# Performance work log

Measured on AMD Instinct MI355X. Metric: run time of the kernel, lower is better.

Reference implementation:

```python
import jax, jax.numpy as jnp
import numpy as np

D_MODEL = 1024
NUM_HEADS = 16
HEAD_DIM = D_MODEL // NUM_HEADS  # 64
THETA = 10000.0
B, S = 2, 2048


def setup_inputs() -> dict:
    key = jax.random.key(0)
    k1, k2, k3 = jax.random.split(key, 3)
    sigma_qkv = (2.0 / (D_MODEL + 3 * D_MODEL)) ** 0.5
    sigma_o = (2.0 / (D_MODEL + D_MODEL)) ** 0.5
    x = jax.random.normal(k1, (B, S, D_MODEL), dtype=jnp.float32)
    w_qkv = jax.random.normal(k2, (3 * D_MODEL, D_MODEL), dtype=jnp.float32) * sigma_qkv
    w_o = jax.random.normal(k3, (D_MODEL, D_MODEL), dtype=jnp.float32) * sigma_o
    token_positions = jnp.arange(S, dtype=jnp.int32)
    return {"x": x, "w_qkv": w_qkv, "w_o": w_o, "token_positions": token_positions, "mask": 1}


def _rope(t, pos):
    # t: (B, H, S, HEAD_DIM); pos: (S,) int
    ids = jnp.arange(HEAD_DIM // 2, dtype=jnp.float32)
    freqs = pos.astype(jnp.float32)[:, None] * (THETA ** (-2.0 * ids / HEAD_DIM))  # (S, HEAD_DIM/2)
    cos, sin = jnp.cos(freqs), jnp.sin(freqs)
    even, odd = t[..., 0::2], t[..., 1::2]
    r_even = even * cos - odd * sin
    r_odd = odd * cos + even * sin
    # interleave back to original layout
    return jnp.stack([r_even, r_odd], axis=-1).reshape(t.shape)


def reference(x, w_qkv, w_o, token_positions, mask):
    # fused QKV projection: Linear computes x @ W^T with W [out, in]
    qkv = x @ w_qkv.T  # (B, S, 3*D_MODEL)
    q, k, v = jnp.split(qkv, 3, axis=-1)

    def to_heads(t):
        return t.reshape(B, S, NUM_HEADS, HEAD_DIM).transpose(0, 2, 1, 3)  # (B, H, S, Dh)

    q, k, v = to_heads(q), to_heads(k), to_heads(v)
    q = _rope(q, token_positions)
    k = _rope(k, token_positions)

    scores = jnp.einsum('bhqd,bhkd->bhqk', q, k)
    if mask:  # causal: lower-triangular allowed
        causal = jnp.tril(jnp.ones((S, S), dtype=bool))
        scores = jnp.where(causal, scores, -jnp.inf)
    attn = jax.nn.softmax(scores * (HEAD_DIM ** -0.5), axis=-1)
    out = jnp.einsum('bhqk,bhkd->bhqd', attn, v)  # (B, H, S, Dh)
    out = out.transpose(0, 2, 1, 3).reshape(B, S, D_MODEL)
    return out @ w_o.T
```

## Files before the change

### kernel.cpp

```cpp
#include <hip/hip_runtime.h>
#include <hip/hip_bf16.h>
#include <math.h>

typedef __bf16 bf16_t;
typedef __bf16 bf16x8 __attribute__((ext_vector_type(8)));
typedef __bf16 bf16x4 __attribute__((ext_vector_type(4)));
typedef float  f32x4  __attribute__((ext_vector_type(4)));

#define D_MODEL 1024
#define NH      16
#define HD      64
#define BATCH   2
#define SEQ     2048
#define MROWS   (BATCH*SEQ)
#define QKVN    (3*D_MODEL)
#define FA_PAD  72
#define SCALE_LOG2E 0.18033688011112042f

__device__ __forceinline__ void async_cp16(const bf16_t* g, bf16_t* l) {
    __builtin_amdgcn_global_load_lds(
        (const __attribute__((address_space(1))) void*)g,
        (__attribute__((address_space(3))) void*)l,
        16, 0, 0);
}

__global__ void cvt_all(const float* __restrict__ x, const float* __restrict__ wq,
                        const float* __restrict__ wo,
                        bf16_t* __restrict__ xb, bf16_t* __restrict__ wqb,
                        bf16_t* __restrict__ wob) {
    const int nx = MROWS * D_MODEL, nq = QKVN * D_MODEL;
    int i = (blockIdx.x * blockDim.x + threadIdx.x) * 4;
    const float* s; bf16_t* d; int off;
    if (i < nx)           { s = x;  d = xb;  off = i; }
    else if (i < nx + nq) { s = wq; d = wqb; off = i - nx; }
    else                  { s = wo; d = wob; off = i - nx - nq; }
    float4 v = *(const float4*)(s + off);
    d[off]     = (bf16_t)v.x;
    d[off + 1] = (bf16_t)v.y;
    d[off + 2] = (bf16_t)v.z;
    d[off + 3] = (bf16_t)v.w;
}

template <typename OutT, int NI>
__global__ __launch_bounds__(256) void gemm_nt(const bf16_t* __restrict__ A,
                                               const bf16_t* __restrict__ Bm,
                                               OutT* __restrict__ C,
                                               int M, int N, int K) {
    __shared__ __align__(16) bf16_t As[128 * 32];
    __shared__ __align__(16) bf16_t Bs[NI * 32 * 32];
    const int tid  = threadIdx.x;
    const int w    = tid >> 6;
    const int lane = tid & 63;
    const int quad = lane >> 4;
    const int l16  = lane & 15;
    const int m0   = blockIdx.x * 128;
    const int n0   = blockIdx.y * (NI * 32);
    const int wm   = (w >> 1) * 64;
    const int wn   = (w & 1) * (NI * 16);

    f32x4 acc[4][NI];
    #pragma unroll
    for (int i = 0; i < 4; i++)
        #pragma unroll
        for (int j = 0; j < NI; j++)
            acc[i][j] = (f32x4){0.f, 0.f, 0.f, 0.f};

    const bf16_t* Ag0 = A  + (size_t)(m0 + (tid >> 2)) * K + (tid & 3) * 8;
    const bf16_t* Ag1 = Ag0 + (size_t)64 * K;
    const bf16_t* Bg0 = Bm + (size_t)(n0 + (tid >> 2)) * K + (tid & 3) * 8;
    const bf16_t* Bg1 = Bg0 + (size_t)64 * K;
    bf16_t* Al0 = &As[(size_t)tid * 8];
    bf16_t* Al1 = &As[((size_t)tid + 256) * 8];
    bf16_t* Bl0 = &Bs[(size_t)tid * 8];
    bf16_t* Bl1 = &Bs[((size_t)tid + 256) * 8];

    for (int k0 = 0; k0 < K; k0 += 32) {
        async_cp16(Ag0 + k0, Al0);
        async_cp16(Ag1 + k0, Al1);
        async_cp16(Bg0 + k0, Bl0);
        if (NI == 4) async_cp16(Bg1 + k0, Bl1);
        __syncthreads();

        bf16x8 af[4], bfr[NI];
        #pragma unroll
        for (int mi = 0; mi < 4; mi++)
            af[mi] = *(const bf16x8*)&As[(wm + mi * 16 + l16) * 32 + quad * 8];
        #pragma unroll
        for (int ni = 0; ni < NI; ni++)
            bfr[ni] = *(const bf16x8*)&Bs[(wn + ni * 16 + l16) * 32 + quad * 8];
        #pragma unroll
        for (int mi = 0; mi < 4; mi++)
            #pragma unroll
            for (int ni = 0; ni < NI; ni++)
                acc[mi][ni] = __builtin_amdgcn_mfma_f32_16x16x32_bf16(
                    af[mi], bfr[ni], acc[mi][ni], 0, 0, 0);
        __syncthreads();
    }

    #pragma unroll
    for (int mi = 0; mi < 4; mi++)
        #pragma unroll
        for (int ni = 0; ni < NI; ni++) {
            const int col = n0 + wn + ni * 16 + l16;
            #pragma unroll
            for (int r = 0; r < 4; r++) {
                const int row = m0 + wm + mi * 16 + quad * 4 + r;
                C[(size_t)row * N + col] = (OutT)acc[mi][ni][r];
            }
        }
}

__global__ __launch_bounds__(256) void rope_split(const bf16_t* __restrict__ qkv,
                                                  const int* __restrict__ pos,
                                                  bf16_t* __restrict__ Qh,
                                                  bf16_t* __restrict__ Kh,
                                                  bf16_t* __restrict__ VT) {
    __shared__ bf16_t vs[128][FA_PAD];
    const int tid   = threadIdx.x;
    const int s_loc = tid >> 1;
    const int half  = tid & 1;
    const int s0    = blockIdx.x * 128;
    const int bh    = blockIdx.y;
    const int b     = bh >> 4, h = bh & 15;
    const int s     = s0 + s_loc;

    const bf16_t* row = qkv + (size_t)(b * SEQ + s) * QKVN + h * HD + half * 32;

    bf16_t qbuf[32], kbuf[32], vbuf[32];
    #pragma unroll
    for (int j = 0; j < 4; j++) {
        *(bf16x8*)&qbuf[j * 8] = *(const bf16x8*)(row + j * 8);
        *(bf16x8*)&kbuf[j * 8] = *(const bf16x8*)(row + D_MODEL + j * 8);
        *(bf16x8*)&vbuf[j * 8] = *(const bf16x8*)(row + 2 * D_MODEL + j * 8);
    }

    const float pf = (float)pos[s];
    #pragma unroll
    for (int p = 0; p < 16; p++) {
        const int d2 = half * 16 + p;
        const float inv = __expf(-0.28782313662425575f * (float)d2);
        const float f = pf * inv;
        const float c = cosf(f), sn = sinf(f);
        float qe = (float)qbuf[2 * p], qo = (float)qbuf[2 * p + 1];
        float ke = (float)kbuf[2 * p], ko = (float)kbuf[2 * p + 1];
        qbuf[2 * p]     = (bf16_t)(qe * c - qo * sn);
        qbuf[2 * p + 1] = (bf16_t)(qo * c + qe * sn);
        kbuf[2 * p]     = (bf16_t)(ke * c - ko * sn);
        kbuf[2 * p + 1] = (bf16_t)(ko * c + ke * sn);
    }

    bf16_t* qdst = Qh + ((size_t)bh * SEQ + s) * HD + half * 32;
    bf16_t* kdst = Kh + ((size_t)bh * SEQ + s) * HD + half * 32;
    #pragma unroll
    for (int j = 0; j < 4; j++) {
        *(bf16x8*)(qdst + j * 8) = *(bf16x8*)&qbuf[j * 8];
        *(bf16x8*)(kdst + j * 8) = *(bf16x8*)&kbuf[j * 8];
        *(bf16x8*)&vs[s_loc][half * 32 + j * 8] = *(bf16x8*)&vbuf[j * 8];
    }
    __syncthreads();

    const int d  = tid >> 2;
    const int sc = tid & 3;
    bf16_t tmp[32];
    #pragma unroll
    for (int i = 0; i < 32; i++) tmp[i] = vs[sc * 32 + i][d];
    bf16_t* vdst = VT + ((size_t)bh * HD + d) * SEQ + s0 + sc * 32;
    #pragma unroll
    for (int j = 0; j < 4; j++)
        *(bf16x8*)(vdst + j * 8) = *(bf16x8*)&tmp[j * 8];
}

__global__ __launch_bounds__(512) void flash_attn(const bf16_t* __restrict__ Qh,
                                                  const bf16_t* __restrict__ Kh,
                                                  const bf16_t* __restrict__ VT,
                                                  bf16_t* __restrict__ AO) {
    __shared__ __align__(16) bf16_t Ks[2][64 * FA_PAD];
    __shared__ __align__(16) bf16_t Vs[2][64 * FA_PAD];
    __shared__ __align__(16) bf16_t pT[8][16][FA_PAD];

    const int tid  = threadIdx.x;
    const int w    = tid >> 6;
    const int lane = tid & 63;
    const int quad = lane >> 4;
    const int l16  = lane & 15;
    const int wq   = w & 3;
    const int g    = w >> 2;

    const int bid  = blockIdx.x;
    const int xcd  = bid & 7;
    const int mm   = bid >> 3;
    const int bh   = (mm >> 4) * 8 + xcd;
    const int pair = mm & 15;
    const int qt_big = 31 - pair;
    const int my_qt  = g ? pair : qt_big;
    const int niter  = qt_big + 1;

    const bf16_t* Qb = Qh + (size_t)bh * SEQ * HD;
    const bf16_t* Kb = Kh + (size_t)bh * SEQ * HD;
    const bf16_t* Vb = VT + (size_t)bh * HD * SEQ;

    const int q0 = my_qt * 64 + wq * 16;
    const bf16x8 aq0 = *(const bf16x8*)(Qb + (size_t)(q0 + l16) * HD + quad * 8);
    const bf16x8 aq1 = *(const bf16x8*)(Qb + (size_t)(q0 + l16) * HD + 32 + quad * 8);

    const int srow = tid >> 3, scol = (tid & 7) * 8;
    const int lds_off = srow * FA_PAD + scol;

    f32x4 o[4];
    #pragma unroll
    for (int i = 0; i < 4; i++) o[i] = (f32x4){0.f, 0.f, 0.f, 0.f};
    float lsum = 0.f;

    bf16x8 pK = *(const bf16x8*)(Kb + (size_t)srow * HD + scol);
    bf16x8 pV = *(const bf16x8*)(Vb + (size_t)srow * SEQ + scol);
    *(bf16x8*)&Ks[0][lds_off] = pK;
    *(bf16x8*)&Vs[0][lds_off] = pV;

    for (int kt = 0; kt < niter; ++kt) {
        const int cur = kt & 1;
        if (kt + 1 < niter) {
            const int kn = (kt + 1) * 64;
            pK = *(const bf16x8*)(Kb + (size_t)(kn + srow) * HD + scol);
            pV = *(const bf16x8*)(Vb + (size_t)srow * SEQ + kn + scol);
        }
        __syncthreads();

        if (kt <= my_qt) {
            const bool diag = (kt == my_qt);
            const bf16_t* KsC = &Ks[cur][0];
            const bf16_t* VsC = &Vs[cur][0];

            #pragma unroll
            for (int ni = 0; ni < 4; ni++) {
                if (diag && ni > wq) {
                    *(bf16x4*)&pT[w][l16][ni * 16 + quad * 4] = (bf16x4){0, 0, 0, 0};
                    continue;
                }
                bf16x8 kb0 = *(const bf16x8*)&KsC[(ni * 16 + l16) * FA_PAD + quad * 8];
                bf16x8 kb1 = *(const bf16x8*)&KsC[(ni * 16 + l16) * FA_PAD + 32 + quad * 8];
                f32x4 t = (f32x4){0.f, 0.f, 0.f, 0.f};
                t = __builtin_amdgcn_mfma_f32_16x16x32_bf16(kb0, aq0, t, 0, 0, 0);
                t = __builtin_amdgcn_mfma_f32_16x16x32_bf16(kb1, aq1, t, 0, 0, 0);
                bf16x4 pk;
                #pragma unroll
                for (int r = 0; r < 4; r++) {
                    float pv = exp2f(t[r] * SCALE_LOG2E);
                    if (diag && (ni * 16 + quad * 4 + r > wq * 16 + l16)) pv = 0.f;
                    lsum += pv;
                    pk[r] = (bf16_t)pv;
                }
                *(bf16x4*)&pT[w][l16][ni * 16 + quad * 4] = pk;
            }

            #pragma unroll
            for (int ks = 0; ks < 2; ks++) {
                if (diag && wq * 16 + 15 < ks * 32) continue;
                bf16x8 ap = *(const bf16x8*)&pT[w][l16][ks * 32 + quad * 8];
                #pragma unroll
                for (int ni = 0; ni < 4; ni++) {
                    bf16x8 vb = *(const bf16x8*)&VsC[(ni * 16 + l16) * FA_PAD + ks * 32 + quad * 8];
                    o[ni] = __builtin_amdgcn_mfma_f32_16x16x32_bf16(ap, vb, o[ni], 0, 0, 0);
                }
            }
        }

        if (kt + 1 < niter) {
            *(bf16x8*)&Ks[cur ^ 1][lds_off] = pK;
            *(bf16x8*)&Vs[cur ^ 1][lds_off] = pV;
        }
    }

    lsum += __shfl_xor(lsum, 16);
    lsum += __shfl_xor(lsum, 32);
    f32x4 linv;
    #pragma unroll
    for (int r = 0; r < 4; r++)
        linv[r] = 1.0f / __shfl(lsum, quad * 4 + r);

    const int b = bh >> 4, h = bh & 15;
    #pragma unroll
    for (int ni = 0; ni < 4; ni++) {
        #pragma unroll
        for (int r = 0; r < 4; r++) {
            const size_t row = (size_t)b * SEQ + q0 + quad * 4 + r;
            AO[row * D_MODEL + h * HD + ni * 16 + l16] = (bf16_t)(o[ni][r] * linv[r]);
        }
    }
}

extern "C" void kernel_launch(void* const* d_in, const int* in_sizes, int n_in,
                              void* d_out, int out_size, void* d_ws, size_t ws_size,
                              hipStream_t stream) {
    const float* x     = (const float*)d_in[0];
    const float* w_qkv = (const float*)d_in[1];
    const float* w_o   = (const float*)d_in[2];
    const int*   tpos  = (const int*)d_in[3];
    float*       out   = (float*)d_out;

    char* ws = (char*)d_ws;
    bf16_t* xb  = (bf16_t*)(ws);
    bf16_t* wqb = (bf16_t*)(ws + 8388608);
    bf16_t* wob = (bf16_t*)(ws + 14680064);
    bf16_t* qkv = (bf16_t*)(ws + 16777216);
    bf16_t* Qh  = (bf16_t*)(ws + 41943040);
    bf16_t* Kh  = (bf16_t*)(ws + 50331648);
    bf16_t* VT  = (bf16_t*)(ws + 58720256);
    bf16_t* AO  = (bf16_t*)(ws + 67108864);

    cvt_all<<<8192, 256, 0, stream>>>(x, w_qkv, w_o, xb, wqb, wob);

    gemm_nt<bf16_t, 4><<<dim3(32, 24), 256, 0, stream>>>(xb, wqb, qkv, MROWS, QKVN, D_MODEL);

    rope_split<<<dim3(SEQ / 128, BATCH * NH), 256, 0, stream>>>(qkv, tpos, Qh, Kh, VT);

    flash_attn<<<512, 512, 0, stream>>>(Qh, Kh, VT, AO);

    gemm_nt<float, 2><<<dim3(32, 16), 256, 0, stream>>>(AO, wob, out, MROWS, D_MODEL, D_MODEL);
}
```

Measured before the change: 201.8 us.

## Split each attention query tile's KV range across two wave groups and merge

Each block now owns a single 64-row query tile, and the two 4-wave groups each process half of the causal KV range. Partial output and row sums are merged through LDS at the end. The old scheme paired a large and a small query tile in one block, so one group often sat idle. The grid doubles to 1024 blocks and the block-to-head mapping changes, at the cost of an extra LDS reduction, an added barrier per iteration, and losing the cross-iteration prefetch double-buffer. Softmax still omits a running max, which is safe only because the two partial sums share no max to rescale.

```diff
diff --git a/kernel.cpp b/kernel.cpp
--- a/kernel.cpp
+++ b/kernel.cpp
@@ -187,19 +187,23 @@
     const int g    = w >> 2;
 
     const int bid  = blockIdx.x;
-    const int xcd  = bid & 7;
-    const int mm   = bid >> 3;
-    const int bh   = (mm >> 4) * 8 + xcd;
-    const int pair = mm & 15;
-    const int qt_big = 31 - pair;
-    const int my_qt  = g ? pair : qt_big;
-    const int niter  = qt_big + 1;
+    const int bh   = bid & 31;
+    const int tb   = bid >> 5;
+    const int u    = tb & 7;
+    const int qtr  = tb >> 3;
+    const int my_t = (qtr == 0) ? (31 - u)
+                   : (qtr == 1) ? (16 + u)
+                   : (qtr == 2) ? (15 - u) : u;
+
+    const int nkv   = my_t + 1;
+    const int h     = nkv >> 1;
+    const int niter = nkv - h;
 
     const bf16_t* Qb = Qh + (size_t)bh * SEQ * HD;
     const bf16_t* Kb = Kh + (size_t)bh * SEQ * HD;
     const bf16_t* Vb = VT + (size_t)bh * HD * SEQ;
 
-    const int q0 = my_qt * 64 + wq * 16;
+    const int q0 = my_t * 64 + wq * 16;
     const bf16x8 aq0 = *(const bf16x8*)(Qb + (size_t)(q0 + l16) * HD + quad * 8);
     const bf16x8 aq1 = *(const bf16x8*)(Qb + (size_t)(q0 + l16) * HD + 32 + quad * 8);
 
@@ -211,24 +215,39 @@
     for (int i = 0; i < 4; i++) o[i] = (f32x4){0.f, 0.f, 0.f, 0.f};
     float lsum = 0.f;
 
-    bf16x8 pK = *(const bf16x8*)(Kb + (size_t)srow * HD + scol);
-    bf16x8 pV = *(const bf16x8*)(Vb + (size_t)srow * SEQ + scol);
-    *(bf16x8*)&Ks[0][lds_off] = pK;
-    *(bf16x8*)&Vs[0][lds_off] = pV;
-
-    for (int kt = 0; kt < niter; ++kt) {
-        const int cur = kt & 1;
-        if (kt + 1 < niter) {
-            const int kn = (kt + 1) * 64;
-            pK = *(const bf16x8*)(Kb + (size_t)(kn + srow) * HD + scol);
-            pV = *(const bf16x8*)(Vb + (size_t)srow * SEQ + kn + scol);
-        }
+    bf16x8 pK0, pV0, pK1, pV1;
+    if (h > 0) {
+        pK0 = *(const bf16x8*)(Kb + (size_t)srow * HD + scol);
+        pV0 = *(const bf16x8*)(Vb + (size_t)srow * SEQ + scol);
+    }
+    pK1 = *(const bf16x8*)(Kb + (size_t)(h * 64 + srow) * HD + scol);
+    pV1 = *(const bf16x8*)(Vb + (size_t)srow * SEQ + h * 64 + scol);
+
+    for (int i = 0; i < niter; ++i) {
+        if (i < h) {
+            *(bf16x8*)&Ks[0][lds_off] = pK0;
+            *(bf16x8*)&Vs[0][lds_off] = pV0;
+        }
+        *(bf16x8*)&Ks[1][lds_off] = pK1;
+        *(bf16x8*)&Vs[1][lds_off] = pV1;
         __syncthreads();
 
-        if (kt <= my_qt) {
-            const bool diag = (kt == my_qt);
-            const bf16_t* KsC = &Ks[cur][0];
-            const bf16_t* VsC = &Vs[cur][0];
+        if (i + 1 < niter) {
+            if (i + 1 < h) {
+                const int k0n = (i + 1) * 64;
+                pK0 = *(const bf16x8*)(Kb + (size_t)(k0n + srow) * HD + scol);
+                pV0 = *(const bf16x8*)(Vb + (size_t)srow * SEQ + k0n + scol);
+            }
+            const int k1n = (h + i + 1) * 64;
+            pK1 = *(const bf16x8*)(Kb + (size_t)(k1n + srow) * HD + scol);
+            pV1 = *(const bf16x8*)(Vb + (size_t)srow * SEQ + k1n + scol);
+        }
+
+        const bool active = g ? true : (i < h);
+        if (active) {
+            const bool diag = g && (i == niter - 1);
+            const bf16_t* KsC = &Ks[g][0];
+            const bf16_t* VsC = &Vs[g][0];
 
             #pragma unroll
             for (int ni = 0; ni < 4; ni++) {
@@ -263,27 +282,39 @@
                 }
             }
         }
-
-        if (kt + 1 < niter) {
-            *(bf16x8*)&Ks[cur ^ 1][lds_off] = pK;
-            *(bf16x8*)&Vs[cur ^ 1][lds_off] = pV;
-        }
-    }
-
-    lsum += __shfl_xor(lsum, 16);
-    lsum += __shfl_xor(lsum, 32);
-    f32x4 linv;
-    #pragma unroll
-    for (int r = 0; r < 4; r++)
-        linv[r] = 1.0f / __shfl(lsum, quad * 4 + r);
-
-    const int b = bh >> 4, h = bh & 15;
-    #pragma unroll
-    for (int ni = 0; ni < 4; ni++) {
-        #pragma unroll
-        for (int r = 0; r < 4; r++) {
-            const size_t row = (size_t)b * SEQ + q0 + quad * 4 + r;
-            AO[row * D_MODEL + h * HD + ni * 16 + l16] = (bf16_t)(o[ni][r] * linv[r]);
+        __syncthreads();
+    }
+
+    f32x4* mo = (f32x4*)&Ks[0][0];
+    float* ml = (float*)(mo + 256 * 4);
+    if (g) {
+        const int base = (wq * 64 + lane) * 4;
+        #pragma unroll
+        for (int ni = 0; ni < 4; ni++) mo[base + ni] = o[ni];
+        ml[wq * 64 + lane] = lsum;
+    }
+    __syncthreads();
+    if (!g) {
+        const int base = (wq * 64 + lane) * 4;
+        #pragma unroll
+        for (int ni = 0; ni < 4; ni++) o[ni] += mo[base + ni];
+        lsum += ml[wq * 64 + lane];
+
+        lsum += __shfl_xor(lsum, 16);
+        lsum += __shfl_xor(lsum, 32);
+        f32x4 linv;
+        #pragma unroll
+        for (int r = 0; r < 4; r++)
+            linv[r] = 1.0f / __shfl(lsum, quad * 4 + r);
+
+        const int b = bh >> 4, hh = bh & 15;
+        #pragma unroll
+        for (int ni = 0; ni < 4; ni++) {
+            #pragma unroll
+            for (int r = 0; r < 4; r++) {
+                const size_t row = (size_t)b * SEQ + q0 + quad * 4 + r;
+                AO[row * D_MODEL + hh * HD + ni * 16 + l16] = (bf16_t)(o[ni][r] * linv[r]);
+            }
         }
     }
 }
@@ -313,7 +344,7 @@
 
     rope_split<<<dim3(SEQ / 128, BATCH * NH), 256, 0, stream>>>(qkv, tpos, Qh, Kh, VT);
 
-    flash_attn<<<512, 512, 0, stream>>>(Qh, Kh, VT, AO);
+    flash_attn<<<1024, 512, 0, stream>>>(Qh, Kh, VT, AO);
 
     gemm_nt<float, 2><<<dim3(32, 16), 256, 0, stream>>>(AO, wob, out, MROWS, D_MODEL, D_MODEL);
 }
```

Measured after the change: 197.0 us. -2.4%, faster.

## Restructure flash attention: per-wave 32-row Q tiles, direct global K/V loads, no block sync

Applied to the files above, without the earlier changes.

The flash attention kernel drops the shared-memory double-buffered K/V tiles and block-wide barriers. Each wave now owns two 16-row query subtiles (32 rows) and reads K and V fragments straight from global memory, relying on L2/cache reuse. Waves in a block get query tiles chosen to balance causal work, and the grid shrinks from 512 to 256 blocks. Removing the barriers lets waves run independently, at the cost of redundant global loads per wave and lower block-level parallelism.

```diff
diff --git a/kernel.cpp b/kernel.cpp
--- a/kernel.cpp
+++ b/kernel.cpp
@@ -174,116 +174,145 @@
                                                   const bf16_t* __restrict__ Kh,
                                                   const bf16_t* __restrict__ VT,
                                                   bf16_t* __restrict__ AO) {
-    __shared__ __align__(16) bf16_t Ks[2][64 * FA_PAD];
-    __shared__ __align__(16) bf16_t Vs[2][64 * FA_PAD];
-    __shared__ __align__(16) bf16_t pT[8][16][FA_PAD];
+    __shared__ __align__(16) bf16_t pT[16][16][FA_PAD];
 
     const int tid  = threadIdx.x;
     const int w    = tid >> 6;
     const int lane = tid & 63;
     const int quad = lane >> 4;
     const int l16  = lane & 15;
-    const int wq   = w & 3;
-    const int g    = w >> 2;
 
     const int bid  = blockIdx.x;
-    const int xcd  = bid & 7;
-    const int mm   = bid >> 3;
-    const int bh   = (mm >> 4) * 8 + xcd;
-    const int pair = mm & 15;
-    const int qt_big = 31 - pair;
-    const int my_qt  = g ? pair : qt_big;
-    const int niter  = qt_big + 1;
+    const int bh   = bid & 31;
+    const int j    = bid >> 5;
+
+    int p;
+    switch (w) {
+        case 0: p = j;      break;
+        case 1: p = 15 - j; break;
+        case 2: p = 16 + j; break;
+        case 3: p = 31 - j; break;
+        case 4: p = 63 - j; break;
+        case 5: p = 48 + j; break;
+        case 6: p = 47 - j; break;
+        default: p = 32 + j;
+    }
+    const int q0   = p * 32;
+    const int nkv  = (q0 + 31) / 64 + 1;
 
     const bf16_t* Qb = Qh + (size_t)bh * SEQ * HD;
     const bf16_t* Kb = Kh + (size_t)bh * SEQ * HD;
     const bf16_t* Vb = VT + (size_t)bh * HD * SEQ;
 
-    const int q0 = my_qt * 64 + wq * 16;
-    const bf16x8 aq0 = *(const bf16x8*)(Qb + (size_t)(q0 + l16) * HD + quad * 8);
-    const bf16x8 aq1 = *(const bf16x8*)(Qb + (size_t)(q0 + l16) * HD + 32 + quad * 8);
-
-    const int srow = tid >> 3, scol = (tid & 7) * 8;
-    const int lds_off = srow * FA_PAD + scol;
-
-    f32x4 o[4];
-    #pragma unroll
-    for (int i = 0; i < 4; i++) o[i] = (f32x4){0.f, 0.f, 0.f, 0.f};
-    float lsum = 0.f;
-
-    bf16x8 pK = *(const bf16x8*)(Kb + (size_t)srow * HD + scol);
-    bf16x8 pV = *(const bf16x8*)(Vb + (size_t)srow * SEQ + scol);
-    *(bf16x8*)&Ks[0][lds_off] = pK;
-    *(bf16x8*)&Vs[0][lds_off] = pV;
-
-    for (int kt = 0; kt < niter; ++kt) {
-        const int cur = kt & 1;
-        if (kt + 1 < niter) {
-            const int kn = (kt + 1) * 64;
-            pK = *(const bf16x8*)(Kb + (size_t)(kn + srow) * HD + scol);
-            pV = *(const bf16x8*)(Vb + (size_t)srow * SEQ + kn + scol);
-        }
-        __syncthreads();
-
-        if (kt <= my_qt) {
-            const bool diag = (kt == my_qt);
-            const bf16_t* KsC = &Ks[cur][0];
-            const bf16_t* VsC = &Vs[cur][0];
-
-            #pragma unroll
-            for (int ni = 0; ni < 4; ni++) {
-                if (diag && ni > wq) {
-                    *(bf16x4*)&pT[w][l16][ni * 16 + quad * 4] = (bf16x4){0, 0, 0, 0};
-                    continue;
-                }
-                bf16x8 kb0 = *(const bf16x8*)&KsC[(ni * 16 + l16) * FA_PAD + quad * 8];
-                bf16x8 kb1 = *(const bf16x8*)&KsC[(ni * 16 + l16) * FA_PAD + 32 + quad * 8];
-                f32x4 t = (f32x4){0.f, 0.f, 0.f, 0.f};
-                t = __builtin_amdgcn_mfma_f32_16x16x32_bf16(kb0, aq0, t, 0, 0, 0);
-                t = __builtin_amdgcn_mfma_f32_16x16x32_bf16(kb1, aq1, t, 0, 0, 0);
-                bf16x4 pk;
-                #pragma unroll
-                for (int r = 0; r < 4; r++) {
-                    float pv = exp2f(t[r] * SCALE_LOG2E);
-                    if (diag && (ni * 16 + quad * 4 + r > wq * 16 + l16)) pv = 0.f;
-                    lsum += pv;
-                    pk[r] = (bf16_t)pv;
-                }
-                *(bf16x4*)&pT[w][l16][ni * 16 + quad * 4] = pk;
-            }
-
-            #pragma unroll
-            for (int ks = 0; ks < 2; ks++) {
-                if (diag && wq * 16 + 15 < ks * 32) continue;
-                bf16x8 ap = *(const bf16x8*)&pT[w][l16][ks * 32 + quad * 8];
+    bf16x8 aq[2][2];
+    #pragma unroll
+    for (int sub = 0; sub < 2; sub++) {
+        aq[sub][0] = *(const bf16x8*)(Qb + (size_t)(q0 + sub * 16 + l16) * HD + quad * 8);
+        aq[sub][1] = *(const bf16x8*)(Qb + (size_t)(q0 + sub * 16 + l16) * HD + 32 + quad * 8);
+    }
+
+    f32x4 o[2][4];
+    #pragma unroll
+    for (int sub = 0; sub < 2; sub++)
+        #pragma unroll
+        for (int i = 0; i < 4; i++) o[sub][i] = (f32x4){0.f, 0.f, 0.f, 0.f};
+    float lsum[2] = {0.f, 0.f};
+
+    for (int kt = 0; kt < nkv; ++kt) {
+        const int kbase = kt * 64;
+
+        bf16x8 kb[4][2];
+        #pragma unroll
+        for (int ni = 0; ni < 4; ni++) {
+            const bf16_t* kr = Kb + (size_t)(kbase + ni * 16 + l16) * HD + quad * 8;
+            kb[ni][0] = *(const bf16x8*)kr;
+            kb[ni][1] = *(const bf16x8*)(kr + 32);
+        }
+
+        const bool full = (kbase + 63 <= q0);
+        if (full) {
+            #pragma unroll
+            for (int sub = 0; sub < 2; sub++) {
+                const int wp = w * 2 + sub;
                 #pragma unroll
                 for (int ni = 0; ni < 4; ni++) {
-                    bf16x8 vb = *(const bf16x8*)&VsC[(ni * 16 + l16) * FA_PAD + ks * 32 + quad * 8];
-                    o[ni] = __builtin_amdgcn_mfma_f32_16x16x32_bf16(ap, vb, o[ni], 0, 0, 0);
+                    f32x4 t = (f32x4){0.f, 0.f, 0.f, 0.f};
+                    t = __builtin_amdgcn_mfma_f32_16x16x32_bf16(kb[ni][0], aq[sub][0], t, 0, 0, 0);
+                    t = __builtin_amdgcn_mfma_f32_16x16x32_bf16(kb[ni][1], aq[sub][1], t, 0, 0, 0);
+                    bf16x4 pk;
+                    #pragma unroll
+                    for (int r = 0; r < 4; r++) {
+                        float pv = exp2f(t[r] * SCALE_LOG2E);
+                        lsum[sub] += pv;
+                        pk[r] = (bf16_t)pv;
+                    }
+                    *(bf16x4*)&pT[wp][l16][ni * 16 + quad * 4] = pk;
                 }
             }
-        }
-
-        if (kt + 1 < niter) {
-            *(bf16x8*)&Ks[cur ^ 1][lds_off] = pK;
-            *(bf16x8*)&Vs[cur ^ 1][lds_off] = pV;
-        }
-    }
-
-    lsum += __shfl_xor(lsum, 16);
-    lsum += __shfl_xor(lsum, 32);
-    f32x4 linv;
-    #pragma unroll
-    for (int r = 0; r < 4; r++)
-        linv[r] = 1.0f / __shfl(lsum, quad * 4 + r);
-
-    const int b = bh >> 4, h = bh & 15;
-    #pragma unroll
-    for (int ni = 0; ni < 4; ni++) {
-        #pragma unroll
-        for (int r = 0; r < 4; r++) {
-            const size_t row = (size_t)b * SEQ + q0 + quad * 4 + r;
-            AO[row * D_MODEL + h * HD + ni * 16 + l16] = (bf16_t)(o[ni][r] * linv[r]);
+        } else {
+            #pragma unroll
+            for (int sub = 0; sub < 2; sub++) {
+                const int wp   = w * 2 + sub;
+                const int qmax = q0 + sub * 16 + 15;
+                const int qg   = q0 + sub * 16 + l16;
+                #pragma unroll
+                for (int ni = 0; ni < 4; ni++) {
+                    if (kbase + ni * 16 > qmax) {
+                        *(bf16x4*)&pT[wp][l16][ni * 16 + quad * 4] = (bf16x4){0, 0, 0, 0};
+                        continue;
+                    }
+                    f32x4 t = (f32x4){0.f, 0.f, 0.f, 0.f};
+                    t = __builtin_amdgcn_mfma_f32_16x16x32_bf16(kb[ni][0], aq[sub][0], t, 0, 0, 0);
+                    t = __builtin_amdgcn_mfma_f32_16x16x32_bf16(kb[ni][1], aq[sub][1], t, 0, 0, 0);
+                    bf16x4 pk;
+                    #pragma unroll
+                    for (int r = 0; r < 4; r++) {
+                        const int kvg = kbase + ni * 16 + quad * 4 + r;
+                        float pv = exp2f(t[r] * SCALE_LOG2E);
+                        if (kvg > qg) pv = 0.f;
+                        lsum[sub] += pv;
+                        pk[r] = (bf16_t)pv;
+                    }
+                    *(bf16x4*)&pT[wp][l16][ni * 16 + quad * 4] = pk;
+                }
+            }
+        }
+
+        #pragma unroll
+        for (int ks = 0; ks < 2; ks++) {
+            if (!full && kbase + ks * 32 > q0 + 31) continue;
+            bf16x8 vb[4];
+            #pragma unroll
+            for (int ni = 0; ni < 4; ni++)
+                vb[ni] = *(const bf16x8*)(Vb + (size_t)(ni * 16 + l16) * SEQ + kbase + ks * 32 + quad * 8);
+            #pragma unroll
+            for (int sub = 0; sub < 2; sub++) {
+                if (!full && kbase + ks * 32 > q0 + sub * 16 + 15) continue;
+                bf16x8 ap = *(const bf16x8*)&pT[w * 2 + sub][l16][ks * 32 + quad * 8];
+                #pragma unroll
+                for (int ni = 0; ni < 4; ni++)
+                    o[sub][ni] = __builtin_amdgcn_mfma_f32_16x16x32_bf16(ap, vb[ni], o[sub][ni], 0, 0, 0);
+            }
+        }
+    }
+
+    const int b = bh >> 4, hh = bh & 15;
+    #pragma unroll
+    for (int sub = 0; sub < 2; sub++) {
+        float ls = lsum[sub];
+        ls += __shfl_xor(ls, 16);
+        ls += __shfl_xor(ls, 32);
+        f32x4 linv;
+        #pragma unroll
+        for (int r = 0; r < 4; r++)
+            linv[r] = 1.0f / __shfl(ls, quad * 4 + r);
+        #pragma unroll
+        for (int ni = 0; ni < 4; ni++) {
+            #pragma unroll
+            for (int r = 0; r < 4; r++) {
+                const size_t row = (size_t)b * SEQ + q0 + sub * 16 + quad * 4 + r;
+                AO[row * D_MODEL + hh * HD + ni * 16 + l16] = (bf16_t)(o[sub][ni][r] * linv[r]);
+            }
         }
     }
 }
@@ -313,7 +342,7 @@
 
     rope_split<<<dim3(SEQ / 128, BATCH * NH), 256, 0, stream>>>(qkv, tpos, Qh, Kh, VT);
 
-    flash_attn<<<512, 512, 0, stream>>>(Qh, Kh, VT, AO);
+    flash_attn<<<256, 512, 0, stream>>>(Qh, Kh, VT, AO);
 
     gemm_nt<float, 2><<<dim3(32, 16), 256, 0, stream>>>(AO, wob, out, MROWS, D_MODEL, D_MODEL);
 }
```

New measurement: 230.2 us. 14.1% more time.

## Split paired-tile flash attention into single-tile 256-thread blocks with single-buffered LDS

Applied to the files above, without the earlier changes.

Each flash-attention block previously held 8 waves working on two query tiles (a long and a short one) that shared K/V loads through a double-buffered LDS ring. It now uses 4 waves per block, one query tile per block, and 1024 blocks ordered from longest to shortest tile. K/V use a single LDS buffer with register prefetch and two barriers per iteration. The aim is to remove the idle waves of the short tile in the paired scheme and to improve occupancy and load balance. In exchange, K/V are loaded from global memory more often and each iteration has an extra barrier.

```diff
diff --git a/kernel.cpp b/kernel.cpp
--- a/kernel.cpp
+++ b/kernel.cpp
@@ -170,104 +170,103 @@
         *(bf16x8*)(vdst + j * 8) = *(bf16x8*)&tmp[j * 8];
 }
 
-__global__ __launch_bounds__(512) void flash_attn(const bf16_t* __restrict__ Qh,
+__global__ __launch_bounds__(256) void flash_attn(const bf16_t* __restrict__ Qh,
                                                   const bf16_t* __restrict__ Kh,
                                                   const bf16_t* __restrict__ VT,
                                                   bf16_t* __restrict__ AO) {
-    __shared__ __align__(16) bf16_t Ks[2][64 * FA_PAD];
-    __shared__ __align__(16) bf16_t Vs[2][64 * FA_PAD];
-    __shared__ __align__(16) bf16_t pT[8][16][FA_PAD];
+    __shared__ __align__(16) bf16_t Ks[64 * FA_PAD];
+    __shared__ __align__(16) bf16_t Vs[64 * FA_PAD];
+    __shared__ __align__(16) bf16_t pT[4][16][FA_PAD];
 
     const int tid  = threadIdx.x;
     const int w    = tid >> 6;
     const int lane = tid & 63;
     const int quad = lane >> 4;
     const int l16  = lane & 15;
-    const int wq   = w & 3;
-    const int g    = w >> 2;
 
     const int bid  = blockIdx.x;
-    const int xcd  = bid & 7;
-    const int mm   = bid >> 3;
-    const int bh   = (mm >> 4) * 8 + xcd;
-    const int pair = mm & 15;
-    const int qt_big = 31 - pair;
-    const int my_qt  = g ? pair : qt_big;
-    const int niter  = qt_big + 1;
+    const int bh   = bid & 31;
+    const int tb   = bid >> 5;
+    const int u    = tb & 7;
+    const int qtr  = tb >> 3;
+    const int my_t = (qtr == 0) ? (31 - u)
+                   : (qtr == 1) ? (16 + u)
+                   : (qtr == 2) ? (15 - u) : u;
+    const int nkv  = my_t + 1;
 
     const bf16_t* Qb = Qh + (size_t)bh * SEQ * HD;
     const bf16_t* Kb = Kh + (size_t)bh * SEQ * HD;
     const bf16_t* Vb = VT + (size_t)bh * HD * SEQ;
 
-    const int q0 = my_qt * 64 + wq * 16;
+    const int q0 = my_t * 64 + w * 16;
     const bf16x8 aq0 = *(const bf16x8*)(Qb + (size_t)(q0 + l16) * HD + quad * 8);
     const bf16x8 aq1 = *(const bf16x8*)(Qb + (size_t)(q0 + l16) * HD + 32 + quad * 8);
 
     const int srow = tid >> 3, scol = (tid & 7) * 8;
-    const int lds_off = srow * FA_PAD + scol;
+    const int lds0 = srow * FA_PAD + scol;
+    const int lds1 = (srow + 32) * FA_PAD + scol;
 
     f32x4 o[4];
     #pragma unroll
     for (int i = 0; i < 4; i++) o[i] = (f32x4){0.f, 0.f, 0.f, 0.f};
     float lsum = 0.f;
 
-    bf16x8 pK = *(const bf16x8*)(Kb + (size_t)srow * HD + scol);
-    bf16x8 pV = *(const bf16x8*)(Vb + (size_t)srow * SEQ + scol);
-    *(bf16x8*)&Ks[0][lds_off] = pK;
-    *(bf16x8*)&Vs[0][lds_off] = pV;
-
-    for (int kt = 0; kt < niter; ++kt) {
-        const int cur = kt & 1;
-        if (kt + 1 < niter) {
+    bf16x8 pK0 = *(const bf16x8*)(Kb + (size_t)srow * HD + scol);
+    bf16x8 pK1 = *(const bf16x8*)(Kb + (size_t)(srow + 32) * HD + scol);
+    bf16x8 pV0 = *(const bf16x8*)(Vb + (size_t)srow * SEQ + scol);
+    bf16x8 pV1 = *(const bf16x8*)(Vb + (size_t)(srow + 32) * SEQ + scol);
+
+    for (int kt = 0; kt < nkv; ++kt) {
+        *(bf16x8*)&Ks[lds0] = pK0;
+        *(bf16x8*)&Ks[lds1] = pK1;
+        *(bf16x8*)&Vs[lds0] = pV0;
+        *(bf16x8*)&Vs[lds1] = pV1;
+        __syncthreads();
+
+        if (kt + 1 < nkv) {
             const int kn = (kt + 1) * 64;
-            pK = *(const bf16x8*)(Kb + (size_t)(kn + srow) * HD + scol);
-            pV = *(const bf16x8*)(Vb + (size_t)srow * SEQ + kn + scol);
-        }
-        __syncthreads();
-
-        if (kt <= my_qt) {
-            const bool diag = (kt == my_qt);
-            const bf16_t* KsC = &Ks[cur][0];
-            const bf16_t* VsC = &Vs[cur][0];
-
+            pK0 = *(const bf16x8*)(Kb + (size_t)(kn + srow) * HD + scol);
+            pK1 = *(const bf16x8*)(Kb + (size_t)(kn + srow + 32) * HD + scol);
+            pV0 = *(const bf16x8*)(Vb + (size_t)srow * SEQ + kn + scol);
+            pV1 = *(const bf16x8*)(Vb + (size_t)(srow + 32) * SEQ + kn + scol);
+        }
+
+        const bool diag = (kt == my_t);
+
+        #pragma unroll
+        for (int ni = 0; ni < 4; ni++) {
+            if (diag && ni > w) {
+                *(bf16x4*)&pT[w][l16][ni * 16 + quad * 4] = (bf16x4){0, 0, 0, 0};
+                continue;
+            }
+            bf16x8 kb0 = *(const bf16x8*)&Ks[(ni * 16 + l16) * FA_PAD + quad * 8];
+            bf16x8 kb1 = *(const bf16x8*)&Ks[(ni * 16 + l16) * FA_PAD + 32 + quad * 8];
+            f32x4 t = (f32x4){0.f, 0.f, 0.f, 0.f};
+            t = __builtin_amdgcn_mfma_f32_16x16x32_bf16(kb0, aq0, t, 0, 0, 0);
+            t = __builtin_amdgcn_mfma_f32_16x16x32_bf16(kb1, aq1, t, 0, 0, 0);
+            bf16x4 pk;
+            #pragma unroll
+            for (int r = 0; r < 4; r++) {
+                float pv = exp2f(t[r] * SCALE_LOG2E);
+                if (diag && (ni * 16 + quad * 4 + r > w * 16 + l16)) pv = 0.f;
+                lsum += pv;
+                pk[r] = (bf16_t)pv;
+            }
+            *(bf16x4*)&pT[w][l16][ni * 16 + quad * 4] = pk;
+        }
+
+        #pragma unroll
+        for (int ks = 0; ks < 2; ks++) {
+            if (diag && w * 16 + 15 < ks * 32) continue;
+            bf16x8 ap = *(const bf16x8*)&pT[w][l16][ks * 32 + quad * 8];
             #pragma unroll
             for (int ni = 0; ni < 4; ni++) {
-                if (diag && ni > wq) {
-                    *(bf16x4*)&pT[w][l16][ni * 16 + quad * 4] = (bf16x4){0, 0, 0, 0};
-                    continue;
-                }
-                bf16x8 kb0 = *(const bf16x8*)&KsC[(ni * 16 + l16) * FA_PAD + quad * 8];
-                bf16x8 kb1 = *(const bf16x8*)&KsC[(ni * 16 + l16) * FA_PAD + 32 + quad * 8];
-                f32x4 t = (f32x4){0.f, 0.f, 0.f, 0.f};
-                t = __builtin_amdgcn_mfma_f32_16x16x32_bf16(kb0, aq0, t, 0, 0, 0);
-                t = __builtin_amdgcn_mfma_f32_16x16x32_bf16(kb1, aq1, t, 0, 0, 0);
-                bf16x4 pk;
-                #pragma unroll
-                for (int r = 0; r < 4; r++) {
-                    float pv = exp2f(t[r] * SCALE_LOG2E);
-                    if (diag && (ni * 16 + quad * 4 + r > wq * 16 + l16)) pv = 0.f;
-                    lsum += pv;
-                    pk[r] = (bf16_t)pv;
-                }
-                *(bf16x4*)&pT[w][l16][ni * 16 + quad * 4] = pk;
+                bf16x8 vb = *(const bf16x8*)&Vs[(ni * 16 + l16) * FA_PAD + ks * 32 + quad * 8];
+                o[ni] = __builtin_amdgcn_mfma_f32_16x16x32_bf16(ap, vb, o[ni], 0, 0, 0);
             }
-
-            #pragma unroll
-            for (int ks = 0; ks < 2; ks++) {
-                if (diag && wq * 16 + 15 < ks * 32) continue;
-                bf16x8 ap = *(const bf16x8*)&pT[w][l16][ks * 32 + quad * 8];
-                #pragma unroll
-                for (int ni = 0; ni < 4; ni++) {
-                    bf16x8 vb = *(const bf16x8*)&VsC[(ni * 16 + l16) * FA_PAD + ks * 32 + quad * 8];
-                    o[ni] = __builtin_amdgcn_mfma_f32_16x16x32_bf16(ap, vb, o[ni], 0, 0, 0);
-                }
-            }
-        }
-
-        if (kt + 1 < niter) {
-            *(bf16x8*)&Ks[cur ^ 1][lds_off] = pK;
-            *(bf16x8*)&Vs[cur ^ 1][lds_off] = pV;
-        }
+        }
+
+        __syncthreads();
     }
 
     lsum += __shfl_xor(lsum, 16);
@@ -277,13 +276,13 @@
     for (int r = 0; r < 4; r++)
         linv[r] = 1.0f / __shfl(lsum, quad * 4 + r);
 
-    const int b = bh >> 4, h = bh & 15;
+    const int b = bh >> 4, hh = bh & 15;
     #pragma unroll
     for (int ni = 0; ni < 4; ni++) {
         #pragma unroll
         for (int r = 0; r < 4; r++) {
             const size_t row = (size_t)b * SEQ + q0 + quad * 4 + r;
-            AO[row * D_MODEL + h * HD + ni * 16 + l16] = (bf16_t)(o[ni][r] * linv[r]);
+            AO[row * D_MODEL + hh * HD + ni * 16 + l16] = (bf16_t)(o[ni][r] * linv[r]);
         }
     }
 }
@@ -313,7 +312,7 @@
 
     rope_split<<<dim3(SEQ / 128, BATCH * NH), 256, 0, stream>>>(qkv, tpos, Qh, Kh, VT);
 
-    flash_attn<<<512, 512, 0, stream>>>(Qh, Kh, VT, AO);
+    flash_attn<<<1024, 256, 0, stream>>>(Qh, Kh, VT, AO);
 
     gemm_nt<float, 2><<<dim3(32, 16), 256, 0, stream>>>(AO, wob, out, MROWS, D_MODEL, D_MODEL);
 }
```

New measurement: 195.2 us. 1.03x faster.
